# Performance work log

Hardware: AMD Instinct MI355X
Metric: run time of the kernel (lower is better)

## Reference

```python
import jax, jax.numpy as jnp
import numpy as np

B, C, H, W = 8, 256, 128, 128
G = 32            # n_groups
CPG = C // G      # channels per group = 8
K = 3             # adaptive spatial kernel and final conv kernel
OUT = 256         # out_channels of final conv
EPS = 1e-5
DN = ('NCHW', 'OIHW', 'NCHW')


def setup_inputs() -> dict:
    key = jax.random.key(0)
    ks = jax.random.split(key, 6)
    x = jax.random.normal(ks[0], (B, C, H, W), jnp.float32)
    w_spatial = jax.random.normal(ks[1], (B, C, CPG, K, K), jnp.float32) * 0.05
    w_pointwise = jax.random.normal(ks[2], (B, C, CPG, 1, 1), jnp.float32) * 0.05
    bias = jax.random.normal(ks[3], (B, C), jnp.float32) * 0.05
    # learned params of the final (static) conv
    conv_w = jax.random.normal(ks[4], (OUT, C, K, K), jnp.float32) * 0.05
    conv_b = jax.random.normal(ks[5], (OUT,), jnp.float32) * 0.05
    return {'x': x, 'w_spatial': w_spatial, 'w_pointwise': w_pointwise,
            'bias': bias, 'conv_w': conv_w, 'conv_b': conv_b}


def _ada_single(x, ws, wp, b):
    # x: [C,H,W]; ws: [C,CPG,K,K]; wp: [C,CPG,1,1]; b: [C]
    pad = (K - 1) // 2
    xp = jnp.pad(x, ((0, 0), (pad, pad), (pad, pad)), mode='reflect')
    # grouped spatial conv (channel-preserving)
    y = jax.lax.conv_general_dilated(
        xp[None], ws, (1, 1), 'VALID',
        dimension_numbers=DN, feature_group_count=G)[0]      # [C,H,W]
    # grouped 1x1 conv as per-group small matmul
    yg = y.reshape(G, CPG, H, W)
    wg = wp[:, :, 0, 0].reshape(G, CPG, CPG)                 # [G, out/g, in/g]
    z = jnp.einsum('goi,gihw->gohw', wg, yg).reshape(C, H, W)
    return z + b[:, None, None]


def reference(x, w_spatial, w_pointwise, bias, conv_w, conv_b):
    # instance norm (no affine), biased variance as in F.instance_norm
    mean = x.mean(axis=(2, 3), keepdims=True)
    var = x.var(axis=(2, 3), keepdims=True)
    xn = (x - mean) * jax.lax.rsqrt(var + EPS)
    # per-sample adaptive depthwise-separable conv
    y = jax.vmap(_ada_single)(xn, w_spatial, w_pointwise, bias)  # [B,C,H,W]
    # final static conv, reflect padding (ceil,floor) = (1,1) for k=3
    yp = jnp.pad(y, ((0, 0), (0, 0), (1, 1), (1, 1)), mode='reflect')
    out = jax.lax.conv_general_dilated(yp, conv_w, (1, 1), 'VALID',
                                       dimension_numbers=DN)
    return out + conv_b[None, :, None, None]
```

## Files before the change

### kernel.cpp

```cpp
#include <hip/hip_runtime.h>
#include <stdint.h>
#include <stddef.h>


typedef __attribute__((ext_vector_type(8))) short   s16x8;
typedef __attribute__((ext_vector_type(4))) float   f32x4;

#define NB   8
#define NC   256
#define NH   128
#define NW   128
#define NG   32
#define CPG  8
#define NOUT 256
#define HWPLANE (NH*NW)

__device__ __forceinline__ unsigned short f2bf(float f) {
    union { float f; unsigned u; } v; v.f = f;
    unsigned u = v.u;
    u += 0x7fffu + ((u >> 16) & 1u);
    return (unsigned short)(u >> 16);
}

__device__ __forceinline__ int refl128(int i) {
    return i < 0 ? 1 : (i > 127 ? 126 : i);
}

__device__ __forceinline__ void async_load16(const void* g, void* l) {
    __builtin_amdgcn_global_load_lds(
        (const __attribute__((address_space(1))) unsigned int*)g,
        (__attribute__((address_space(3))) unsigned int*)l,
        16, 0, 0);
}

__global__ __launch_bounds__(256) void stats_k(const float* __restrict__ x,
                                               float* __restrict__ stats) {
    int bc = blockIdx.x, t = threadIdx.x;
    const float4* p = (const float4*)(x + (size_t)bc * HWPLANE);
    float s = 0.f, q = 0.f;
#pragma unroll
    for (int k = 0; k < 16; ++k) {
        float4 v = p[k * 256 + t];
        s += v.x + v.y + v.z + v.w;
        q += v.x * v.x + v.y * v.y + v.z * v.z + v.w * v.w;
    }
    __shared__ float ss[256], sq[256];
    ss[t] = s; sq[t] = q;
    __syncthreads();
    for (int o = 128; o > 0; o >>= 1) {
        if (t < o) { ss[t] += ss[t + o]; sq[t] += sq[t + o]; }
        __syncthreads();
    }
    if (t == 0) {
        float mean = ss[0] * (1.f / HWPLANE);
        float var  = sq[0] * (1.f / HWPLANE) - mean * mean;
        stats[bc * 2]     = mean;
        stats[bc * 2 + 1] = rsqrtf(var + 1e-5f);
    }
}

__global__ __launch_bounds__(256) void wfrag_k(const float* __restrict__ wsp,
                                               const float* __restrict__ wpw,
                                               const float* __restrict__ bias,
                                               unsigned short* __restrict__ wfrag,
                                               float* __restrict__ bias16) {
    int tid = blockIdx.x * 256 + threadIdx.x;
    if (tid < 49152) {
        int lane = tid & 63;
        int kw   = (tid >> 6) % 3;
        int bg   = tid / 192;
        int oc   = lane & 15;
        int tap  = kw * 4 + (lane >> 4);
        unsigned short fr[8];
#pragma unroll
        for (int e = 0; e < 8; ++e) {
            float v = 0.f;
            if (tap < 9 && oc < 8) {
#pragma unroll
                for (int j = 0; j < 8; ++j)
                    v += wpw[(bg * 8 + oc) * 8 + j] *
                         wsp[((bg * 8 + j) * 8 + e) * 9 + tap];
            }
            fr[e] = f2bf(v);
        }
        uint4 pk;
        pk.x = (unsigned)fr[0] | ((unsigned)fr[1] << 16);
        pk.y = (unsigned)fr[2] | ((unsigned)fr[3] << 16);
        pk.z = (unsigned)fr[4] | ((unsigned)fr[5] << 16);
        pk.w = (unsigned)fr[6] | ((unsigned)fr[7] << 16);
        *(uint4*)(wfrag + (size_t)((bg * 3 + kw) * 64 + lane) * 8) = pk;
    } else {
        int t2 = tid - 49152;
        int bg = t2 >> 4, j = t2 & 15;
        bias16[bg * 16 + j] = (j < 8) ? bias[bg * 8 + j] : 0.f;
    }
}

__global__ __launch_bounds__(256) void repack_k(const float* __restrict__ cw,
                                                unsigned short* __restrict__ wtT) {
    __shared__ float ld[2304];
    const int blk = blockIdx.x;
    const float* src = cw + (size_t)blk * 2304;
#pragma unroll
    for (int it = 0; it < 9; ++it)
        ld[it * 256 + threadIdx.x] = src[it * 256 + threadIdx.x];
    __syncthreads();
    int p = blk * 256 + threadIdx.x;
    int o = p >> 8, c = p & 255;
#pragma unroll
    for (int t = 0; t < 9; ++t)
        wtT[((size_t)t * NOUT + o) * NC + c] = f2bf(ld[threadIdx.x * 9 + t]);
}

__global__ __launch_bounds__(256) void ada_k(const float* __restrict__ x,
                                             const float* __restrict__ stats,
                                             const unsigned short* __restrict__ wfrag,
                                             const float* __restrict__ bias16,
                                             unsigned short* __restrict__ z) {
    __shared__ s16x8 tile[34 * 128];
    const int id = blockIdx.x;
    const int b  = id & 7;
    const int g  = (id >> 3) & 31;
    const int q  = id >> 8;
    const int bg = b * 32 + g;
    const int h0 = q * 32;

    const int tid  = threadIdx.x;
    const int lane = tid & 63;
    const int wv   = tid >> 6;
    const int l15  = lane & 15;
    const int quad = lane >> 4;

    float mean[8], rstd[8];
#pragma unroll
    for (int ic = 0; ic < 8; ++ic) {
        mean[ic] = stats[(bg * 8 + ic) * 2];
        rstd[ic] = stats[(bg * 8 + ic) * 2 + 1];
    }

    const float* xg = x + (size_t)bg * 8 * HWPLANE;
#pragma unroll
    for (int it = 0; it < 17; ++it) {
        int slot = it * 256 + tid;
        int row  = slot >> 7;
        int w    = slot & 127;
        int gr   = refl128(h0 - 1 + row);
        const float* xp = xg + gr * NW + w;
        unsigned short u[8];
#pragma unroll
        for (int ic = 0; ic < 8; ++ic)
            u[ic] = f2bf((xp[(size_t)ic * HWPLANE] - mean[ic]) * rstd[ic]);
        uint4 pk;
        pk.x = (unsigned)u[0] | ((unsigned)u[1] << 16);
        pk.y = (unsigned)u[2] | ((unsigned)u[3] << 16);
        pk.z = (unsigned)u[4] | ((unsigned)u[5] << 16);
        pk.w = (unsigned)u[6] | ((unsigned)u[7] << 16);
        *(uint4*)&tile[slot] = pk;
    }
    __syncthreads();

    s16x8 wf[3];
#pragma unroll
    for (int kw = 0; kw < 3; ++kw)
        wf[kw] = *(const s16x8*)(wfrag + (size_t)((bg * 3 + kw) * 64 + lane) * 8);
    float4 bv = *(const float4*)(bias16 + bg * 16 + quad * 4);

    int dhA[3], dwm[3];
#pragma unroll
    for (int kw = 0; kw < 3; ++kw) {
        int tap = kw * 4 + quad;
        if (tap < 9) { dhA[kw] = tap / 3; dwm[kw] = tap % 3 - 1; }
        else         { dhA[kw] = 0;       dwm[kw] = 0; }
    }

#pragma unroll 2
    for (int i = 0; i < 64; ++i) {
        int pb = wv * 64 + i;
        int ro = pb >> 3;
        int w0 = (pb & 7) * 16;
        f32x4 acc = {};
#pragma unroll
        for (int kw = 0; kw < 3; ++kw) {
            int wr = refl128(w0 + l15 + dwm[kw]);
            s16x8 xf = tile[(ro + dhA[kw]) * 128 + wr];
            acc = __builtin_amdgcn_mfma_f32_16x16x32_bf16(wf[kw], xf, acc, 0, 0, 0);
        }
        unsigned short o0 = f2bf(acc[0] + bv.x);
        unsigned short o1 = f2bf(acc[1] + bv.y);
        unsigned short o2 = f2bf(acc[2] + bv.z);
        unsigned short o3 = f2bf(acc[3] + bv.w);
        if (lane < 32) {
            uint2 pk2 = { (unsigned)o0 | ((unsigned)o1 << 16),
                          (unsigned)o2 | ((unsigned)o3 << 16) };
            unsigned short* zp = z + ((size_t)(bg * NH + h0 + ro) * NW + w0 + l15) * 8
                                   + quad * 4;
            *(uint2*)zp = pk2;
        }
    }
}

__global__ __launch_bounds__(256) void final_k(const unsigned short* __restrict__ z,
                                               const unsigned short* __restrict__ wtT,
                                               const float* __restrict__ cb,
                                               float* __restrict__ out) {
    __shared__ s16x8 sAv[1024];
    __shared__ s16x8 sBv[2][1024];

    const int id = blockIdx.x;
    const int b  = id & 7;
    const int jb = id >> 3;
    const int nb = jb & 1;
    const int h  = jb >> 1;

    const int tid  = threadIdx.x;
    const int wv   = tid >> 6;
    const int lane = tid & 63;
    const int l15  = lane & 15;
    const int quad = lane >> 4;
    const int mo   = (wv & 1) << 6;
    const int nol  = (wv >> 1) << 6;
    const int n0   = (nb << 7) + nol;

    int srcB[4], ldsoff[4];
#pragma unroll
    for (int it = 0; it < 4; ++it) {
        int ch  = it * 256 + tid;
        int row = ch >> 3, cp = ch & 7;
        srcB[it]   = row * 512 + ((cp ^ (row & 7)) << 4);
        ldsoff[it] = it * 256 + wv * 64;
    }

    int srcA[4];
#pragma unroll
    for (int it = 0; it < 4; ++it) {
        int ch = it * 256 + tid;
        int gq = ch >> 7, wslot = ch & 127;
        srcA[it] = gq * 262144 + ((wslot ^ (gq & 7)) << 4);
    }

    int aoff[3][4][2];
#pragma unroll
    for (int dw = 0; dw < 3; ++dw)
#pragma unroll
        for (int i = 0; i < 4; ++i) {
            int w_ = refl128(mo + 16 * i + l15 + dw - 1);
#pragma unroll
            for (int kk = 0; kk < 2; ++kk) {
                int gq = kk * 4 + quad;
                aoff[dw][i][kk] = gq * 128 + (w_ ^ (gq & 7));
            }
        }
    int boff[4][2];
#pragma unroll
    for (int j = 0; j < 4; ++j) {
        int oc_l = nol + 16 * j + l15;
#pragma unroll
        for (int kk = 0; kk < 2; ++kk)
            boff[j][kk] = oc_l * 8 + ((kk * 4 + quad) ^ (oc_l & 7));
    }

    const char* zb = (const char*)z + (size_t)b * (NG * NH * NW * CPG * 2);
    const char* zr[3];
#pragma unroll
    for (int dh = 0; dh < 3; ++dh)
        zr[dh] = zb + (size_t)refl128(h + dh - 1) * (NW * CPG * 2);
    const char* wt = (const char*)wtT + nb * 65536;

    auto stageA = [&](const char* g) {
#pragma unroll
        for (int it = 0; it < 4; ++it)
            async_load16(g + srcA[it], (void*)(sAv + ldsoff[it]));
    };
    auto stageB = [&](const char* g, int bsel) {
#pragma unroll
        for (int it = 0; it < 4; ++it)
            async_load16(g + srcB[it], (void*)(sBv[bsel] + ldsoff[it]));
    };

    f32x4 acc[4][4] = {};

    auto compute = [&](const int (&ao)[4][2], int bsel) {
        const s16x8* bbase = sBv[bsel];
#pragma unroll
        for (int kk = 0; kk < 2; ++kk) {
            s16x8 av[4], bv[4];
#pragma unroll
            for (int i = 0; i < 4; ++i) av[i] = sAv[ao[i][kk]];
#pragma unroll
            for (int j = 0; j < 4; ++j) bv[j] = bbase[boff[j][kk]];
#pragma unroll
            for (int i = 0; i < 4; ++i)
#pragma unroll
                for (int j = 0; j < 4; ++j)
                    acc[i][j] = __builtin_amdgcn_mfma_f32_16x16x32_bf16(
                        av[i], bv[j], acc[i][j], 0, 0, 0);
        }
    };

    int buf = 0;
    stageA(zr[0]);
    stageB(wt, 0);
    __syncthreads();

    for (int sc = 0; sc < 12; ++sc) {
        const int dh = sc >> 2, kc = sc & 3;
        const char* bt = wt + (size_t)(dh * 3) * 131072 + kc * 128;
        stageB(bt + 131072, buf ^ 1);
        compute(aoff[0], buf);
        __syncthreads(); buf ^= 1;
        stageB(bt + 262144, buf ^ 1);
        compute(aoff[1], buf);
        __syncthreads(); buf ^= 1;
        compute(aoff[2], buf);
        __syncthreads();
        if (sc < 11) {
            const int sn = sc + 1, dhn = sn >> 2, kcn = sn & 3;
            stageA(zr[dhn] + (size_t)kcn * 2097152);
            stageB(wt + (size_t)(dhn * 3) * 131072 + kcn * 128, buf ^ 1);
            __syncthreads();
        }
        buf ^= 1;
    }

#pragma unroll
    for (int j = 0; j < 4; ++j) {
        int oc = n0 + 16 * j + l15;
        float bvl = cb[oc];
#pragma unroll
        for (int i = 0; i < 4; ++i) {
            int w0 = mo + 16 * i + quad * 4;
            float* dst = out + (((size_t)(b * NOUT + oc) * NH + h) * NW + w0);
            f32x4 v = acc[i][j];
            float4 o4 = { v[0] + bvl, v[1] + bvl, v[2] + bvl, v[3] + bvl };
            *(float4*)dst = o4;
        }
    }
}

extern "C" void kernel_launch(void* const* d_in, const int* in_sizes, int n_in,
                              void* d_out, int out_size, void* d_ws, size_t ws_size,
                              hipStream_t stream) {
    const float* x   = (const float*)d_in[0];
    const float* wsp = (const float*)d_in[1];
    const float* wpw = (const float*)d_in[2];
    const float* bia = (const float*)d_in[3];
    const float* cw  = (const float*)d_in[4];
    const float* cb  = (const float*)d_in[5];
    float* out = (float*)d_out;

    char* ws = (char*)d_ws;
    float*          stats  = (float*)ws;
    unsigned short* wfrag  = (unsigned short*)(ws + 16384);
    float*          bias16 = (float*)(ws + 802816);
    unsigned short* wtT    = (unsigned short*)(ws + 819200);
    unsigned short* z      = (unsigned short*)(ws + 1998848);

    stats_k <<<NB * NC, 256, 0, stream>>>(x, stats);
    wfrag_k <<<208,     256, 0, stream>>>(wsp, wpw, bia, wfrag, bias16);
    repack_k<<<256,     256, 0, stream>>>(cw, wtT);
    ada_k   <<<NB * NG * 4, 256, 0, stream>>>(x, stats, wfrag, bias16, z);
    final_k <<<NB * NH * 2, 256, 0, stream>>>(z, wtT, cb, out);
}
```

Measured before the change: 438.3 us.

## Fold instance-norm into adaptive weights and bias, fuse stats with bf16 cast

Replaces the separate stats pass with a kernel that reads x once, accumulates per-channel sums via atomics, and writes a raw bf16 channel-interleaved copy. The normalization is folded algebraically into the adaptive conv: weights are scaled by rstd at load time and the mean term becomes a bias correction using precomputed tap-summed weights. The ada kernel then streams the bf16 tile into LDS with async global-to-LDS loads instead of normalizing fp32 x on the fly, and the final kernel gets an occupancy hint. It adds a large workspace buffer, a memset, batch chunking when workspace is small, and some precision change because un-normalized values are rounded to bf16.

```diff
diff --git a/kernel.cpp b/kernel.cpp
--- a/kernel.cpp
+++ b/kernel.cpp
@@ -33,37 +33,71 @@
         16, 0, 0);
 }
 
-__global__ __launch_bounds__(256) void stats_k(const float* __restrict__ x,
-                                               float* __restrict__ stats) {
-    int bc = blockIdx.x, t = threadIdx.x;
-    const float4* p = (const float4*)(x + (size_t)bc * HWPLANE);
-    float s = 0.f, q = 0.f;
-#pragma unroll
-    for (int k = 0; k < 16; ++k) {
-        float4 v = p[k * 256 + t];
-        s += v.x + v.y + v.z + v.w;
-        q += v.x * v.x + v.y * v.y + v.z * v.z + v.w * v.w;
-    }
-    __shared__ float ss[256], sq[256];
-    ss[t] = s; sq[t] = q;
+__global__ __launch_bounds__(256) void castz_k(const float* __restrict__ x,
+                                               float* __restrict__ sacc,
+                                               unsigned short* __restrict__ xn,
+                                               int b0, int nbloc, int lognb) {
+    const int id = blockIdx.x;
+    const int bl = id & (nbloc - 1);
+    const int g  = (id >> lognb) & 31;
+    const int qh = id >> (lognb + 5);
+    const int bgG = (b0 + bl) * 32 + g;
+    const int bgL = bl * 32 + g;
+    const int tid = threadIdx.x;
+    const int lane = tid & 63;
+    const int wv   = tid >> 6;
+
+    const size_t pb  = (size_t)bgG * 8 * HWPLANE + qh * 4096;
+    unsigned short* xq = xn + ((size_t)bgL * HWPLANE + qh * 4096) * 8;
+
+    float s[8] = {}, q2[8] = {};
+#pragma unroll 4
+    for (int i = 0; i < 16; ++i) {
+        int pix = i * 256 + tid;
+        unsigned short u[8];
+#pragma unroll
+        for (int ic = 0; ic < 8; ++ic) {
+            float v = x[pb + (size_t)ic * HWPLANE + pix];
+            s[ic] += v; q2[ic] += v * v;
+            u[ic] = f2bf(v);
+        }
+        uint4 pk;
+        pk.x = (unsigned)u[0] | ((unsigned)u[1] << 16);
+        pk.y = (unsigned)u[2] | ((unsigned)u[3] << 16);
+        pk.z = (unsigned)u[4] | ((unsigned)u[5] << 16);
+        pk.w = (unsigned)u[6] | ((unsigned)u[7] << 16);
+        *(uint4*)(xq + (size_t)pix * 8) = pk;
+    }
+#pragma unroll
+    for (int o = 32; o; o >>= 1) {
+#pragma unroll
+        for (int ic = 0; ic < 8; ++ic) {
+            s[ic]  += __shfl_xor(s[ic],  o, 64);
+            q2[ic] += __shfl_xor(q2[ic], o, 64);
+        }
+    }
+    __shared__ float red[4][16];
+    if (lane == 0) {
+#pragma unroll
+        for (int ic = 0; ic < 8; ++ic) {
+            red[wv][ic * 2]     = s[ic];
+            red[wv][ic * 2 + 1] = q2[ic];
+        }
+    }
     __syncthreads();
-    for (int o = 128; o > 0; o >>= 1) {
-        if (t < o) { ss[t] += ss[t + o]; sq[t] += sq[t + o]; }
-        __syncthreads();
-    }
-    if (t == 0) {
-        float mean = ss[0] * (1.f / HWPLANE);
-        float var  = sq[0] * (1.f / HWPLANE) - mean * mean;
-        stats[bc * 2]     = mean;
-        stats[bc * 2 + 1] = rsqrtf(var + 1e-5f);
+    if (tid < 16) {
+        float t = red[0][tid] + red[1][tid] + red[2][tid] + red[3][tid];
+        int ic = tid >> 1, sel = tid & 1;
+        atomicAdd(&sacc[((size_t)bgG * 8 + ic) * 2 + sel], t);
     }
 }
 
 __global__ __launch_bounds__(256) void wfrag_k(const float* __restrict__ wsp,
                                                const float* __restrict__ wpw,
                                                const float* __restrict__ bias,
-                                               unsigned short* __restrict__ wfrag,
-                                               float* __restrict__ bias16) {
+                                               float* __restrict__ wfragF,
+                                               float* __restrict__ bias16,
+                                               float* __restrict__ S) {
     int tid = blockIdx.x * 256 + threadIdx.x;
     if (tid < 49152) {
         int lane = tid & 63;
@@ -71,7 +105,7 @@
         int bg   = tid / 192;
         int oc   = lane & 15;
         int tap  = kw * 4 + (lane >> 4);
-        unsigned short fr[8];
+        float fr[8];
 #pragma unroll
         for (int e = 0; e < 8; ++e) {
             float v = 0.f;
@@ -81,18 +115,33 @@
                     v += wpw[(bg * 8 + oc) * 8 + j] *
                          wsp[((bg * 8 + j) * 8 + e) * 9 + tap];
             }
-            fr[e] = f2bf(v);
-        }
-        uint4 pk;
-        pk.x = (unsigned)fr[0] | ((unsigned)fr[1] << 16);
-        pk.y = (unsigned)fr[2] | ((unsigned)fr[3] << 16);
-        pk.z = (unsigned)fr[4] | ((unsigned)fr[5] << 16);
-        pk.w = (unsigned)fr[6] | ((unsigned)fr[7] << 16);
-        *(uint4*)(wfrag + (size_t)((bg * 3 + kw) * 64 + lane) * 8) = pk;
-    } else {
+            fr[e] = v;
+        }
+        float* dst = wfragF + (size_t)((bg * 3 + kw) * 64 + lane) * 8;
+        *(float4*)dst       = make_float4(fr[0], fr[1], fr[2], fr[3]);
+        *(float4*)(dst + 4) = make_float4(fr[4], fr[5], fr[6], fr[7]);
+    } else if (tid < 53248) {
         int t2 = tid - 49152;
         int bg = t2 >> 4, j = t2 & 15;
         bias16[bg * 16 + j] = (j < 8) ? bias[bg * 8 + j] : 0.f;
+    } else {
+        int t3 = tid - 53248;
+        int ic = t3 & 7;
+        int oc = (t3 >> 3) & 15;
+        int bg = t3 >> 7;
+        float v = 0.f;
+        if (oc < 8) {
+#pragma unroll
+            for (int j = 0; j < 8; ++j) {
+                float wj = wpw[(bg * 8 + oc) * 8 + j];
+                float ts = 0.f;
+#pragma unroll
+                for (int tap = 0; tap < 9; ++tap)
+                    ts += wsp[((bg * 8 + j) * 8 + ic) * 9 + tap];
+                v += wj * ts;
+            }
+        }
+        S[(size_t)(bg * 16 + oc) * 8 + ic] = v;
     }
 }
 
@@ -112,17 +161,20 @@
         wtT[((size_t)t * NOUT + o) * NC + c] = f2bf(ld[threadIdx.x * 9 + t]);
 }
 
-__global__ __launch_bounds__(256) void ada_k(const float* __restrict__ x,
-                                             const float* __restrict__ stats,
-                                             const unsigned short* __restrict__ wfrag,
+__global__ __launch_bounds__(256) void ada_k(const unsigned short* __restrict__ xn,
+                                             const float* __restrict__ sacc,
+                                             const float* __restrict__ wfragF,
                                              const float* __restrict__ bias16,
-                                             unsigned short* __restrict__ z) {
+                                             const float* __restrict__ S,
+                                             unsigned short* __restrict__ z,
+                                             int b0, int nbloc, int lognb) {
     __shared__ s16x8 tile[34 * 128];
     const int id = blockIdx.x;
-    const int b  = id & 7;
-    const int g  = (id >> 3) & 31;
-    const int q  = id >> 8;
-    const int bg = b * 32 + g;
+    const int bl = id & (nbloc - 1);
+    const int g  = (id >> lognb) & 31;
+    const int q  = id >> (lognb + 5);
+    const int bgG = (b0 + bl) * 32 + g;
+    const int bgL = bl * 32 + g;
     const int h0 = q * 32;
 
     const int tid  = threadIdx.x;
@@ -131,39 +183,59 @@
     const int l15  = lane & 15;
     const int quad = lane >> 4;
 
-    float mean[8], rstd[8];
+    const char* xnbg = (const char*)xn + (size_t)bgL * HWPLANE * 16;
+    {
+        const int rsub = tid >> 7;
+        const int wcol = tid & 127;
+#pragma unroll
+        for (int it = 0; it < 17; ++it) {
+            int r  = it * 2 + rsub;
+            int gr = refl128(h0 - 1 + r);
+            const char* src = xnbg + (size_t)gr * 2048 + wcol * 16;
+            async_load16(src, (void*)(tile + it * 256 + wv * 64));
+        }
+    }
+
+    float rst[8], msr[8];
 #pragma unroll
     for (int ic = 0; ic < 8; ++ic) {
-        mean[ic] = stats[(bg * 8 + ic) * 2];
-        rstd[ic] = stats[(bg * 8 + ic) * 2 + 1];
-    }
-
-    const float* xg = x + (size_t)bg * 8 * HWPLANE;
-#pragma unroll
-    for (int it = 0; it < 17; ++it) {
-        int slot = it * 256 + tid;
-        int row  = slot >> 7;
-        int w    = slot & 127;
-        int gr   = refl128(h0 - 1 + row);
-        const float* xp = xg + gr * NW + w;
-        unsigned short u[8];
-#pragma unroll
-        for (int ic = 0; ic < 8; ++ic)
-            u[ic] = f2bf((xp[(size_t)ic * HWPLANE] - mean[ic]) * rstd[ic]);
-        uint4 pk;
-        pk.x = (unsigned)u[0] | ((unsigned)u[1] << 16);
-        pk.y = (unsigned)u[2] | ((unsigned)u[3] << 16);
-        pk.z = (unsigned)u[4] | ((unsigned)u[5] << 16);
-        pk.w = (unsigned)u[6] | ((unsigned)u[7] << 16);
-        *(uint4*)&tile[slot] = pk;
-    }
-    __syncthreads();
+        float sm = sacc[((size_t)bgG * 8 + ic) * 2];
+        float sq = sacc[((size_t)bgG * 8 + ic) * 2 + 1];
+        float mean = sm * (1.f / HWPLANE);
+        float var  = sq * (1.f / HWPLANE) - mean * mean;
+        float r = rsqrtf(var + 1e-5f);
+        rst[ic] = r;
+        msr[ic] = mean * r;
+    }
 
     s16x8 wf[3];
 #pragma unroll
-    for (int kw = 0; kw < 3; ++kw)
-        wf[kw] = *(const s16x8*)(wfrag + (size_t)((bg * 3 + kw) * 64 + lane) * 8);
-    float4 bv = *(const float4*)(bias16 + bg * 16 + quad * 4);
+    for (int kw = 0; kw < 3; ++kw) {
+        const float* wp = wfragF + (size_t)((bgG * 3 + kw) * 64 + lane) * 8;
+        float4 a = *(const float4*)wp;
+        float4 c = *(const float4*)(wp + 4);
+        unsigned short e0 = f2bf(a.x * rst[0]), e1 = f2bf(a.y * rst[1]);
+        unsigned short e2 = f2bf(a.z * rst[2]), e3 = f2bf(a.w * rst[3]);
+        unsigned short e4 = f2bf(c.x * rst[4]), e5 = f2bf(c.y * rst[5]);
+        unsigned short e6 = f2bf(c.z * rst[6]), e7 = f2bf(c.w * rst[7]);
+        union { uint4 u; s16x8 v; } pk;
+        pk.u.x = (unsigned)e0 | ((unsigned)e1 << 16);
+        pk.u.y = (unsigned)e2 | ((unsigned)e3 << 16);
+        pk.u.z = (unsigned)e4 | ((unsigned)e5 << 16);
+        pk.u.w = (unsigned)e6 | ((unsigned)e7 << 16);
+        wf[kw] = pk.v;
+    }
+
+    float badj[4];
+#pragma unroll
+    for (int r = 0; r < 4; ++r) {
+        int oc = quad * 4 + r;
+        const float* sp = S + (size_t)(bgG * 16 + oc) * 8;
+        float a = bias16[bgG * 16 + oc];
+#pragma unroll
+        for (int ic = 0; ic < 8; ++ic) a -= msr[ic] * sp[ic];
+        badj[r] = a;
+    }
 
     int dhA[3], dwm[3];
 #pragma unroll
@@ -172,6 +244,8 @@
         if (tap < 9) { dhA[kw] = tap / 3; dwm[kw] = tap % 3 - 1; }
         else         { dhA[kw] = 0;       dwm[kw] = 0; }
     }
+
+    __syncthreads();
 
 #pragma unroll 2
     for (int i = 0; i < 64; ++i) {
@@ -185,24 +259,24 @@
             s16x8 xf = tile[(ro + dhA[kw]) * 128 + wr];
             acc = __builtin_amdgcn_mfma_f32_16x16x32_bf16(wf[kw], xf, acc, 0, 0, 0);
         }
-        unsigned short o0 = f2bf(acc[0] + bv.x);
-        unsigned short o1 = f2bf(acc[1] + bv.y);
-        unsigned short o2 = f2bf(acc[2] + bv.z);
-        unsigned short o3 = f2bf(acc[3] + bv.w);
+        unsigned short o0 = f2bf(acc[0] + badj[0]);
+        unsigned short o1 = f2bf(acc[1] + badj[1]);
+        unsigned short o2 = f2bf(acc[2] + badj[2]);
+        unsigned short o3 = f2bf(acc[3] + badj[3]);
         if (lane < 32) {
             uint2 pk2 = { (unsigned)o0 | ((unsigned)o1 << 16),
                           (unsigned)o2 | ((unsigned)o3 << 16) };
-            unsigned short* zp = z + ((size_t)(bg * NH + h0 + ro) * NW + w0 + l15) * 8
+            unsigned short* zp = z + ((size_t)(bgG * NH + h0 + ro) * NW + w0 + l15) * 8
                                    + quad * 4;
             *(uint2*)zp = pk2;
         }
     }
 }
 
-__global__ __launch_bounds__(256) void final_k(const unsigned short* __restrict__ z,
-                                               const unsigned short* __restrict__ wtT,
-                                               const float* __restrict__ cb,
-                                               float* __restrict__ out) {
+__global__ __launch_bounds__(256, 3) void final_k(const unsigned short* __restrict__ z,
+                                                  const unsigned short* __restrict__ wtT,
+                                                  const float* __restrict__ cb,
+                                                  float* __restrict__ out) {
     __shared__ s16x8 sAv[1024];
     __shared__ s16x8 sBv[2][1024];
 
@@ -349,15 +423,25 @@
     float* out = (float*)d_out;
 
     char* ws = (char*)d_ws;
-    float*          stats  = (float*)ws;
-    unsigned short* wfrag  = (unsigned short*)(ws + 16384);
-    float*          bias16 = (float*)(ws + 802816);
-    unsigned short* wtT    = (unsigned short*)(ws + 819200);
-    unsigned short* z      = (unsigned short*)(ws + 1998848);
-
-    stats_k <<<NB * NC, 256, 0, stream>>>(x, stats);
-    wfrag_k <<<208,     256, 0, stream>>>(wsp, wpw, bia, wfrag, bias16);
-    repack_k<<<256,     256, 0, stream>>>(cw, wtT);
-    ada_k   <<<NB * NG * 4, 256, 0, stream>>>(x, stats, wfrag, bias16, z);
+    float*          sacc   = (float*)ws;
+    float*          wfragF = (float*)(ws + 16384);
+    float*          bias16 = (float*)(ws + 1589248);
+    float*          S      = (float*)(ws + 1605632);
+    unsigned short* wtT    = (unsigned short*)(ws + 1736704);
+    unsigned short* z      = (unsigned short*)(ws + 2916352);
+    unsigned short* xn     = (unsigned short*)(ws + 70025216);
+
+    int nbloc = 8, lognb = 3;
+    while (nbloc > 1 &&
+           70025216ull + (size_t)nbloc * 16777216ull > ws_size) { nbloc >>= 1; --lognb; }
+
+    hipMemsetAsync(sacc, 0, 16384, stream);
+    wfrag_k <<<336, 256, 0, stream>>>(wsp, wpw, bia, wfragF, bias16, S);
+    repack_k<<<256, 256, 0, stream>>>(cw, wtT);
+    for (int b0 = 0; b0 < NB; b0 += nbloc) {
+        castz_k<<<nbloc * 128, 256, 0, stream>>>(x, sacc, xn, b0, nbloc, lognb);
+        ada_k  <<<nbloc * 128, 256, 0, stream>>>(xn, sacc, wfragF, bias16, S, z,
+                                                 b0, nbloc, lognb);
+    }
     final_k <<<NB * NH * 2, 256, 0, stream>>>(z, wtT, cb, out);
 }
```

Result: faster. 425.3 us (-3.0%).
